# Kernel tuning notes

Measured on AMD Instinct MI355X. Metric: run time of the kernel, lower is better.

The kernel has to match this reference:

```python
import jax, jax.numpy as jnp
import numpy as np

WORD_THRES = 0.2
COS_EPS = 1e-8
NEG_INF = -1e9


def setup_inputs() -> dict:
    key = jax.random.key(0)
    k1, k2, k3, k4 = jax.random.split(key, 4)
    B, L, V, E, A = 1024, 256, 50000, 300, 30
    inputs = jax.random.randint(k1, (B, L), 0, V)            # token ids, 0 == pad
    w_emb = jax.random.normal(k2, (V, E), dtype=jnp.float32) * 0.1
    a_emb = jax.random.normal(k3, (A, E), dtype=jnp.float32)
    a_weight = jax.random.uniform(k4, (A,), dtype=jnp.float32)
    return {"inputs": inputs, "w_emb": w_emb, "a_emb": a_emb, "a_weight": a_weight}


def reference(inputs, w_emb, a_emb, a_weight):
    # inputs: [B, L] int ids; w_emb: [V, E]; a_emb: [A, E]; a_weight: [A]
    inputs_len = (inputs != 0).sum(axis=1).astype(jnp.float32)      # [B]
    x_wrd = w_emb[inputs]                                            # [B, L, E]

    # cosine similarity between each aspect and each word (torch semantics:
    # dot / (max(||a||, eps) * max(||x||, eps)))
    a_norm = jnp.maximum(jnp.linalg.norm(a_emb, axis=-1), COS_EPS)   # [A]
    x_norm = jnp.maximum(jnp.linalg.norm(x_wrd, axis=-1), COS_EPS)   # [B, L]
    dot = jnp.einsum("ae,ble->abl", a_emb, x_wrd)                    # [A, B, L]
    sim = dot / (a_norm[:, None, None] * x_norm[None, :, :])

    # Threshold(word_thres, 0): x if x > thres else 0, then scale by aspect weight
    sim = jnp.where(sim > WORD_THRES, sim, 0.0) * a_weight[:, None, None]

    # centroid score: relu(sim).max over aspects, summed over seq, length-normalized
    centroid = jnp.maximum(sim, 0.0).max(axis=0)                     # [B, L]
    centroid_score = centroid.sum(axis=1) / (inputs_len + 1e-5)      # [B]

    # attention: mask exact zeros to -1e9, max over aspects, softmax over seq
    sim_m = jnp.where(sim == 0.0, NEG_INF, sim)
    scores = sim_m.max(axis=0)                                       # [B, L]
    a = jax.nn.softmax(scores, axis=1)                               # [B, L]

    z = jnp.einsum("bl,ble->be", a, x_wrd)                           # [B, E]
    enc_out = z * (centroid_score > 1e-4).astype(z.dtype)[:, None]
    return enc_out, a, centroid_score
```

## Files before the change

kernel.cpp:

```cpp
#include <hip/hip_runtime.h>
#include <math.h>

#define BB 1024
#define LL 256
#define VV 50000
#define EE 300
#define AA 30
#define WORD_THRES 0.2f
#define COS_EPS_F 1e-8f
#define NEG_INF_F -1e9f

__global__ void __launch_bounds__(256) cent_kernel(
    const float* __restrict__ w_emb,
    const float* __restrict__ a_emb,
    const float* __restrict__ a_weight,
    float* __restrict__ cent)
{
    __shared__ float4 s_a[AA * 75];
    __shared__ float s_scale[AA];
    __shared__ float s_aw[AA];

    const int t = threadIdx.x;
    const float4* __restrict__ a4 = (const float4*)a_emb;

    for (int s = t; s < AA * 75; s += 256) s_a[s] = a4[s];

    {
        const int a = t >> 3, j = t & 7;
        if (a < AA) {
            float n2a = 0.f;
            for (int c = j; c < 75; c += 8) {
                const float4 x = a4[a * 75 + c];
                n2a += x.x * x.x + x.y * x.y + x.z * x.z + x.w * x.w;
            }
            n2a += __shfl_xor(n2a, 1);
            n2a += __shfl_xor(n2a, 2);
            n2a += __shfl_xor(n2a, 4);
            if (j == 0) {
                s_scale[a] = 1.f / fmaxf(sqrtf(n2a), COS_EPS_F);
                s_aw[a] = a_weight[a];
            }
        }
    }
    __syncthreads();

    const int p = t & 3;
    const int slot = t >> 2;
    const int v0 = blockIdx.x * 128 + slot;
    const int v1 = v0 + 64;
    const bool ok1 = v1 < VV;
    const float* __restrict__ r0 = w_emb + (size_t)v0 * EE;
    const float* __restrict__ r1 = w_emb + (size_t)(ok1 ? v1 : 0) * EE;

    float acc0[AA], acc1[AA];
#pragma unroll
    for (int a = 0; a < AA; ++a) { acc0[a] = 0.f; acc1[a] = 0.f; }
    float n20 = 0.f, n21 = 0.f;

    for (int k = 0; k < 18; ++k) {
        const int j = 4 * k + p;
        const float4 w0 = *(const float4*)(r0 + 4 * j);
        const float4 w1 = *(const float4*)(r1 + 4 * j);
        n20 += w0.x * w0.x + w0.y * w0.y + w0.z * w0.z + w0.w * w0.w;
        n21 += w1.x * w1.x + w1.y * w1.y + w1.z * w1.z + w1.w * w1.w;
        const float4* __restrict__ ap = s_a + j;
#pragma unroll
        for (int a = 0; a < AA; ++a) {
            const float4 av = ap[a * 75];
            acc0[a] = fmaf(av.x, w0.x, fmaf(av.y, w0.y,
                      fmaf(av.z, w0.z, fmaf(av.w, w0.w, acc0[a]))));
            acc1[a] = fmaf(av.x, w1.x, fmaf(av.y, w1.y,
                      fmaf(av.z, w1.z, fmaf(av.w, w1.w, acc1[a]))));
        }
    }
    if (p < 3) {
        const int j = 72 + p;
        const float4 w0 = *(const float4*)(r0 + 4 * j);
        const float4 w1 = *(const float4*)(r1 + 4 * j);
        n20 += w0.x * w0.x + w0.y * w0.y + w0.z * w0.z + w0.w * w0.w;
        n21 += w1.x * w1.x + w1.y * w1.y + w1.z * w1.z + w1.w * w1.w;
        const float4* __restrict__ ap = s_a + j;
#pragma unroll
        for (int a = 0; a < AA; ++a) {
            const float4 av = ap[a * 75];
            acc0[a] = fmaf(av.x, w0.x, fmaf(av.y, w0.y,
                      fmaf(av.z, w0.z, fmaf(av.w, w0.w, acc0[a]))));
            acc1[a] = fmaf(av.x, w1.x, fmaf(av.y, w1.y,
                      fmaf(av.z, w1.z, fmaf(av.w, w1.w, acc1[a]))));
        }
    }

#pragma unroll
    for (int a = 0; a < AA; ++a) {
        acc0[a] += __shfl_xor(acc0[a], 1); acc0[a] += __shfl_xor(acc0[a], 2);
        acc1[a] += __shfl_xor(acc1[a], 1); acc1[a] += __shfl_xor(acc1[a], 2);
    }
    n20 += __shfl_xor(n20, 1); n20 += __shfl_xor(n20, 2);
    n21 += __shfl_xor(n21, 1); n21 += __shfl_xor(n21, 2);

    if (p == 0) {
        const float inv_x0 = 1.f / fmaxf(sqrtf(n20), COS_EPS_F);
        const float inv_x1 = 1.f / fmaxf(sqrtf(n21), COS_EPS_F);
        float m0 = 0.f, m1 = 0.f;
#pragma unroll
        for (int a = 0; a < AA; ++a) {
            const float c0 = acc0[a] * s_scale[a] * inv_x0;
            const float c1 = acc1[a] * s_scale[a] * inv_x1;
            m0 = fmaxf(m0, (c0 > WORD_THRES) ? c0 * s_aw[a] : 0.f);
            m1 = fmaxf(m1, (c1 > WORD_THRES) ? c1 * s_aw[a] : 0.f);
        }
        cent[v0] = m0;
        if (ok1) cent[v1] = m1;
    }
}

__global__ void __launch_bounds__(256) row_kernel(
    const int* __restrict__ inputs,
    const float* __restrict__ w_emb,
    const float* __restrict__ cent,
    float* __restrict__ out)
{
    const int b = blockIdx.x;
    const int t = threadIdx.x;
    const int wid = t >> 6, lane = t & 63;

    __shared__ float pA[4], pB[4], pC[4], pD[4];
    __shared__ int s_nact;
    __shared__ int s_act_id[LL];
    __shared__ float s_act_w[LL];

    const int id = inputs[b * LL + t];
    const float c = cent[id];
    const float score = (c > 0.f) ? c : NEG_INF_F;
    const float cnt = (id != 0) ? 1.f : 0.f;
    if (t == 0) s_nact = 0;

    float s1 = c, s2 = cnt, s3 = score;
#pragma unroll
    for (int o = 32; o > 0; o >>= 1) {
        s1 += __shfl_down(s1, o);
        s2 += __shfl_down(s2, o);
        s3 = fmaxf(s3, __shfl_down(s3, o));
    }
    if (lane == 0) { pA[wid] = s1; pB[wid] = s2; pC[wid] = s3; }
    __syncthreads();

    const float sum_c = pA[0] + pA[1] + pA[2] + pA[3];
    const float len   = pB[0] + pB[1] + pB[2] + pB[3];
    const float mx    = fmaxf(fmaxf(pC[0], pC[1]), fmaxf(pC[2], pC[3]));

    const float p = expf(score - mx);
    float s4 = p;
#pragma unroll
    for (int o = 32; o > 0; o >>= 1) s4 += __shfl_down(s4, o);
    if (lane == 0) pD[wid] = s4;
    __syncthreads();
    const float sum_p = pD[0] + pD[1] + pD[2] + pD[3];

    const float a_l = p / sum_p;
    const float cs = sum_c / (len + 1e-5f);
    const float gate = (cs > 1e-4f) ? 1.f : 0.f;

    out[BB * EE + b * LL + t] = a_l;
    if (t == 0) out[BB * EE + BB * LL + b] = cs;

    if (score > -1e8f) {
        const int i = atomicAdd(&s_nact, 1);
        s_act_id[i] = id;
        s_act_w[i] = a_l;
    }
    __syncthreads();
    const int n = s_nact;

    if (t < EE / 4) {
        float4 acc = {0.f, 0.f, 0.f, 0.f};
        for (int i = 0; i < n; ++i) {
            const float wgt = s_act_w[i];
            const float4 r = *(const float4*)(w_emb + (size_t)s_act_id[i] * EE + 4 * t);
            acc.x += wgt * r.x; acc.y += wgt * r.y;
            acc.z += wgt * r.z; acc.w += wgt * r.w;
        }
        acc.x *= gate; acc.y *= gate; acc.z *= gate; acc.w *= gate;
        *(float4*)(out + b * EE + 4 * t) = acc;
    }
}

extern "C" void kernel_launch(void* const* d_in, const int* in_sizes, int n_in,
                              void* d_out, int out_size, void* d_ws, size_t ws_size,
                              hipStream_t stream) {
    const int* inputs = (const int*)d_in[0];
    const float* w_emb = (const float*)d_in[1];
    const float* a_emb = (const float*)d_in[2];
    const float* a_weight = (const float*)d_in[3];
    float* out = (float*)d_out;
    float* cent = (float*)d_ws;

    cent_kernel<<<(VV + 127) / 128, 256, 0, stream>>>(w_emb, a_emb, a_weight, cent);
    row_kernel<<<BB, 256, 0, stream>>>(inputs, w_emb, cent, out);
}
```

Baseline: 125.2 us.

## Retile cent_kernel: split aspects across lanes and register-block four vocab rows

Changes the per-vocab centroid kernel's work split. Each thread now covers 15 of the 30 aspects for 4 vocab rows, with 8 lanes splitting the embedding dimension, instead of all 30 aspects for 2 rows with 4 lanes. Each shared-memory aspect load is reused across four rows, raising FMA-per-LDS and cutting the accumulator count per thread from 60 to 60 in a different shape. The cost is more shuffle reduction steps, an extra cross-half max shuffle, idle lanes on the tail iteration, and twice as many blocks, each reloading the aspect table.

```diff
diff --git a/kernel.cpp b/kernel.cpp
--- a/kernel.cpp
+++ b/kernel.cpp
@@ -44,73 +44,80 @@
     }
     __syncthreads();
 
-    const int p = t & 3;
-    const int slot = t >> 2;
-    const int v0 = blockIdx.x * 128 + slot;
-    const int v1 = v0 + 64;
-    const bool ok1 = v1 < VV;
-    const float* __restrict__ r0 = w_emb + (size_t)v0 * EE;
-    const float* __restrict__ r1 = w_emb + (size_t)(ok1 ? v1 : 0) * EE;
-
-    float acc0[AA], acc1[AA];
-#pragma unroll
-    for (int a = 0; a < AA; ++a) { acc0[a] = 0.f; acc1[a] = 0.f; }
-    float n20 = 0.f, n21 = 0.f;
-
-    for (int k = 0; k < 18; ++k) {
-        const int j = 4 * k + p;
-        const float4 w0 = *(const float4*)(r0 + 4 * j);
-        const float4 w1 = *(const float4*)(r1 + 4 * j);
-        n20 += w0.x * w0.x + w0.y * w0.y + w0.z * w0.z + w0.w * w0.w;
-        n21 += w1.x * w1.x + w1.y * w1.y + w1.z * w1.z + w1.w * w1.w;
-        const float4* __restrict__ ap = s_a + j;
-#pragma unroll
-        for (int a = 0; a < AA; ++a) {
-            const float4 av = ap[a * 75];
-            acc0[a] = fmaf(av.x, w0.x, fmaf(av.y, w0.y,
-                      fmaf(av.z, w0.z, fmaf(av.w, w0.w, acc0[a]))));
-            acc1[a] = fmaf(av.x, w1.x, fmaf(av.y, w1.y,
-                      fmaf(av.z, w1.z, fmaf(av.w, w1.w, acc1[a]))));
-        }
-    }
-    if (p < 3) {
-        const int j = 72 + p;
-        const float4 w0 = *(const float4*)(r0 + 4 * j);
-        const float4 w1 = *(const float4*)(r1 + 4 * j);
-        n20 += w0.x * w0.x + w0.y * w0.y + w0.z * w0.z + w0.w * w0.w;
-        n21 += w1.x * w1.x + w1.y * w1.y + w1.z * w1.z + w1.w * w1.w;
-        const float4* __restrict__ ap = s_a + j;
-#pragma unroll
-        for (int a = 0; a < AA; ++a) {
-            const float4 av = ap[a * 75];
-            acc0[a] = fmaf(av.x, w0.x, fmaf(av.y, w0.y,
-                      fmaf(av.z, w0.z, fmaf(av.w, w0.w, acc0[a]))));
-            acc1[a] = fmaf(av.x, w1.x, fmaf(av.y, w1.y,
-                      fmaf(av.z, w1.z, fmaf(av.w, w1.w, acc1[a]))));
-        }
-    }
-
-#pragma unroll
-    for (int a = 0; a < AA; ++a) {
-        acc0[a] += __shfl_xor(acc0[a], 1); acc0[a] += __shfl_xor(acc0[a], 2);
-        acc1[a] += __shfl_xor(acc1[a], 1); acc1[a] += __shfl_xor(acc1[a], 2);
-    }
-    n20 += __shfl_xor(n20, 1); n20 += __shfl_xor(n20, 2);
-    n21 += __shfl_xor(n21, 1); n21 += __shfl_xor(n21, 2);
-
-    if (p == 0) {
-        const float inv_x0 = 1.f / fmaxf(sqrtf(n20), COS_EPS_F);
-        const float inv_x1 = 1.f / fmaxf(sqrtf(n21), COS_EPS_F);
-        float m0 = 0.f, m1 = 0.f;
-#pragma unroll
-        for (int a = 0; a < AA; ++a) {
-            const float c0 = acc0[a] * s_scale[a] * inv_x0;
-            const float c1 = acc1[a] * s_scale[a] * inv_x1;
-            m0 = fmaxf(m0, (c0 > WORD_THRES) ? c0 * s_aw[a] : 0.f);
-            m1 = fmaxf(m1, (c1 > WORD_THRES) ? c1 * s_aw[a] : 0.f);
-        }
-        cent[v0] = m0;
-        if (ok1) cent[v1] = m1;
+    const int p    = t & 7;
+    const int ah   = (t >> 3) & 1;
+    const int slot = t >> 4;
+    const int a_base = ah * 15;
+
+    const float* __restrict__ r[4];
+    bool ok[4];
+#pragma unroll
+    for (int i = 0; i < 4; ++i) {
+        const int v = blockIdx.x * 64 + slot + 16 * i;
+        ok[i] = v < VV;
+        r[i] = w_emb + (size_t)(ok[i] ? v : 0) * EE;
+    }
+
+    float acc[15][4];
+#pragma unroll
+    for (int a = 0; a < 15; ++a)
+#pragma unroll
+        for (int i = 0; i < 4; ++i) acc[a][i] = 0.f;
+    float n2[4] = {0.f, 0.f, 0.f, 0.f};
+
+    for (int k = 0; k < 10; ++k) {
+        const int j = 8 * k + p;
+        if (j < 75) {
+            float4 wv[4];
+#pragma unroll
+            for (int i = 0; i < 4; ++i) {
+                wv[i] = *(const float4*)(r[i] + 4 * j);
+                n2[i] += wv[i].x * wv[i].x + wv[i].y * wv[i].y +
+                         wv[i].z * wv[i].z + wv[i].w * wv[i].w;
+            }
+            const float4* __restrict__ ap = s_a + a_base * 75 + j;
+#pragma unroll
+            for (int a = 0; a < 15; ++a) {
+                const float4 av = ap[a * 75];
+#pragma unroll
+                for (int i = 0; i < 4; ++i) {
+                    acc[a][i] = fmaf(av.x, wv[i].x, fmaf(av.y, wv[i].y,
+                                fmaf(av.z, wv[i].z, fmaf(av.w, wv[i].w, acc[a][i]))));
+                }
+            }
+        }
+    }
+
+#pragma unroll
+    for (int i = 0; i < 4; ++i) {
+        n2[i] += __shfl_xor(n2[i], 1);
+        n2[i] += __shfl_xor(n2[i], 2);
+        n2[i] += __shfl_xor(n2[i], 4);
+#pragma unroll
+        for (int a = 0; a < 15; ++a) {
+            acc[a][i] += __shfl_xor(acc[a][i], 1);
+            acc[a][i] += __shfl_xor(acc[a][i], 2);
+            acc[a][i] += __shfl_xor(acc[a][i], 4);
+        }
+    }
+
+    float m[4] = {0.f, 0.f, 0.f, 0.f};
+#pragma unroll
+    for (int i = 0; i < 4; ++i) {
+        const float invx = 1.f / fmaxf(sqrtf(n2[i]), COS_EPS_F);
+#pragma unroll
+        for (int a = 0; a < 15; ++a) {
+            const float cosv = acc[a][i] * s_scale[a_base + a] * invx;
+            m[i] = fmaxf(m[i], (cosv > WORD_THRES) ? cosv * s_aw[a_base + a] : 0.f);
+        }
+    }
+#pragma unroll
+    for (int i = 0; i < 4; ++i) m[i] = fmaxf(m[i], __shfl_xor(m[i], 8));
+
+    if (p == 0 && ah == 0) {
+#pragma unroll
+        for (int i = 0; i < 4; ++i)
+            if (ok[i]) cent[blockIdx.x * 64 + slot + 16 * i] = m[i];
     }
 }
 
@@ -176,9 +183,9 @@
         float4 acc = {0.f, 0.f, 0.f, 0.f};
         for (int i = 0; i < n; ++i) {
             const float wgt = s_act_w[i];
-            const float4 r = *(const float4*)(w_emb + (size_t)s_act_id[i] * EE + 4 * t);
-            acc.x += wgt * r.x; acc.y += wgt * r.y;
-            acc.z += wgt * r.z; acc.w += wgt * r.w;
+            const float4 rr = *(const float4*)(w_emb + (size_t)s_act_id[i] * EE + 4 * t);
+            acc.x += wgt * rr.x; acc.y += wgt * rr.y;
+            acc.z += wgt * rr.z; acc.w += wgt * rr.w;
         }
         acc.x *= gate; acc.y *= gate; acc.z *= gate; acc.w *= gate;
         *(float4*)(out + b * EE + 4 * t) = acc;
@@ -195,6 +202,6 @@
     float* out = (float*)d_out;
     float* cent = (float*)d_ws;
 
-    cent_kernel<<<(VV + 127) / 128, 256, 0, stream>>>(w_emb, a_emb, a_weight, cent);
+    cent_kernel<<<(VV + 63) / 64, 256, 0, stream>>>(w_emb, a_emb, a_weight, cent);
     row_kernel<<<BB, 256, 0, stream>>>(inputs, w_emb, cent, out);
 }
```

New measurement: 126.9 us. No clear change (+1.3%).
